# Kernel optimization log

Measured on AMD Instinct MI355X. Metric: run time of the kernel, lower is better.

Reference implementation:

```python
import jax, jax.numpy as jnp
import numpy as np


def _aggregate(xyz, node, features, k):
    # xyz: [B,3,N], node: [B,3,M], features: [B,C,N] -> [B,C,M]
    # squared euclidean distances via expansion (same math as (x-n)^2 sum)
    d = (jnp.sum(xyz ** 2, axis=1)[:, :, None]
         + jnp.sum(node ** 2, axis=1)[:, None, :]
         - 2.0 * jnp.einsum('bdn,bdm->bnm', xyz, node))  # [B,N,M]
    # k smallest over N for each of M nodes (order irrelevant: max-pool after)
    _, nn_idx = jax.lax.top_k(-jnp.transpose(d, (0, 2, 1)), k)  # [B,M,k]
    # gather C-channel features at neighbor indices -> [B,C,M,k]
    g = jnp.take_along_axis(features[:, :, None, :], nn_idx[:, None, :, :], axis=3)
    return jnp.max(g, axis=3)  # [B,C,M]


def setup_inputs() -> dict:
    key = jax.random.key(0)
    k1, k2, k3, k4 = jax.random.split(key, 4)
    B, N, C = 4, 16384, 128
    return {
        'input_coords': jax.random.normal(k1, (B, 3, N), dtype=jnp.float32),
        'input_feats': jax.random.normal(k2, (B, C, N), dtype=jnp.float32),
        'W': jax.random.normal(k3, (C, C), dtype=jnp.float32) * 0.05,
        'b': jax.random.normal(k4, (C,), dtype=jnp.float32) * 0.05,
        'num_sample': 2048,
        'num_agg': 16,
    }


def reference(input_coords, input_feats, W, b, num_sample, num_agg):
    # Dropout in eval mode -> identity. proj = 1x1 Conv1d == per-point linear.
    Z = input_feats  # [B,C,N]
    proj = jax.nn.relu(jnp.einsum('oc,bcn->bon', W, Z) + b[None, :, None])
    vector = jnp.max(proj, axis=-1, keepdims=True)  # [B,C,1]
    weights = jnp.sum(input_feats * vector, axis=1)  # [B,N]
    scores = jax.nn.sigmoid(weights)
    values, idx = jax.lax.top_k(scores, num_sample)  # [B,M] each, sorted desc
    pool_coords_static = jnp.take_along_axis(input_coords, idx[:, None, :], axis=2)  # [B,3,M]
    pool_feats_static = jnp.take_along_axis(input_feats, idx[:, None, :], axis=2)    # [B,C,M]
    v = values[:, None, :]  # [B,1,M]
    pool_feats = pool_feats_static * v
    pool_coords = pool_coords_static * v
    agg_feats = _aggregate(input_coords, pool_coords_static, input_feats, num_agg)  # [B,C,M]
    pool_feats = jnp.concatenate([pool_feats, agg_feats], axis=1)  # [B,2C,M]
    return (pool_coords_static, pool_coords, pool_feats)
```

## Files before the change

kernel.cpp:

```cpp
#include <hip/hip_runtime.h>
#include <hip/hip_bf16.h>
#include <stdint.h>

#define BB 4
#define NN 16384
#define CC 128
#define MM 2048
#define KNN 16
#define QCAP 512
#define EPS 1e-3f

typedef unsigned int u32;
typedef unsigned short u16;
typedef unsigned long long u64;

#define OFF_FEATT   0ull
#define OFF_PTS4    33554432ull
#define OFF_WT      37748736ull
#define OFF_KEYS    37814272ull
#define OFF_VEC     38338560ull
#define OFF_IDX     38340608ull
#define OFF_VAL     38373376ull
#define OFF_TMP1    38406144ull
#define OFF_TMP2    38668288ull

__device__ __forceinline__ float np_dist(float4 p, float4 nd) {
#pragma clang fp contract(off)
    float dot = ((p.x * nd.x) + (p.y * nd.y)) + (p.z * nd.z);
    float d = (p.w + nd.w) - 2.0f * dot;
    return d;
}

__device__ __forceinline__ float sfast(float4 p, float4 nd) {
    float dot = fmaf(p.x, nd.x, fmaf(p.y, nd.y, p.z * nd.z));
    return fmaf(-2.0f, dot, p.w);
}

__device__ __forceinline__ u32 mono_bits(float d) {
    u32 u = __float_as_uint(d);
    u ^= ((u32)(((int)u) >> 31)) | 0x80000000u;
    return u;
}

__device__ __forceinline__ float kth16(float v, int l) {
    float sv = v;
#pragma unroll
    for (int k = 2; k <= 64; k <<= 1) {
#pragma unroll
        for (int j = k >> 1; j > 0; j >>= 1) {
            float pv = __shfl_xor(sv, j);
            bool up = ((l & k) == 0);
            bool tmin = (((l & j) == 0) == up);
            float mn = fminf(sv, pv), mx = fmaxf(sv, pv);
            sv = tmin ? mn : mx;
        }
    }
    return __shfl(sv, 15);
}

__global__ void k_prep(const float* __restrict__ coords, const float* __restrict__ W,
                       float4* __restrict__ pts4, float* __restrict__ WT,
                       u32* __restrict__ vecU) {
    int g = blockIdx.x * 256 + threadIdx.x;
    if (g < BB * NN) {
        int b = g >> 14, n = g & (NN - 1);
        const float* cb = coords + (size_t)b * 3 * NN;
        float x = cb[n], y = cb[NN + n], z = cb[2 * NN + n];
        float w;
        {
#pragma clang fp contract(off)
            w = ((x * x) + (y * y)) + (z * z);
        }
        pts4[g] = make_float4(x, y, z, w);
    } else if (g < BB * NN + CC * CC) {
        int i = g - BB * NN;
        int o = i >> 7, c = i & 127;
        WT[c * CC + o] = W[i];
    } else if (g < BB * NN + CC * CC + BB * CC) {
        vecU[g - BB * NN - CC * CC] = 0u;
    }
}

__global__ __launch_bounds__(256) void k_tv(const float* __restrict__ feats,
        const float* __restrict__ WT, const float* __restrict__ bias,
        float* __restrict__ feat_t, u32* __restrict__ vecU) {
    __shared__ float t[CC][65];
    int bx = blockIdx.x;
    int b = bx >> 8; int n0 = (bx & 255) * 64;
    int tid = threadIdx.x, l = tid & 63;
    int w = __builtin_amdgcn_readfirstlane(tid >> 6);
    const float* fb = feats + (size_t)b * CC * NN + n0;
#pragma unroll
    for (int p = 0; p < 32; ++p) {
        int r = p * 4 + w;
        t[r][l] = fb[(size_t)r * NN + l];
    }
    __syncthreads();
    float* ob = feat_t + ((size_t)b * NN + n0) * CC;
#pragma unroll
    for (int p = 0; p < 32; ++p) {
        int r = (p >> 1) * 4 + w;
        int c = (p & 1) * 64 + l;
        ob[(size_t)r * CC + c] = t[c][r];
    }
    int o0 = w * 32;
    float acc[32];
#pragma unroll
    for (int oi = 0; oi < 32; ++oi) acc[oi] = bias[o0 + oi];
    for (int c = 0; c < CC; ++c) {
        float zc = t[c][l];
        const float4* wt4 = (const float4*)(WT + c * CC + o0);
#pragma unroll
        for (int q = 0; q < 8; ++q) {
            float4 wv = wt4[q];
            acc[q * 4 + 0] = fmaf(wv.x, zc, acc[q * 4 + 0]);
            acc[q * 4 + 1] = fmaf(wv.y, zc, acc[q * 4 + 1]);
            acc[q * 4 + 2] = fmaf(wv.z, zc, acc[q * 4 + 2]);
            acc[q * 4 + 3] = fmaf(wv.w, zc, acc[q * 4 + 3]);
        }
    }
#pragma unroll
    for (int oi = 0; oi < 32; ++oi) {
        float rv = acc[oi] > 0.0f ? acc[oi] : 0.0f;
#pragma unroll
        for (int s = 32; s; s >>= 1) rv = fmaxf(rv, __shfl_xor(rv, s));
        if (l == 0) atomicMax(vecU + b * CC + o0 + oi, __float_as_uint(rv));
    }
}

__global__ void k_scores(const float* __restrict__ feats, const float* __restrict__ vecF,
                         u64* __restrict__ keys) {
    int i = blockIdx.x * 256 + threadIdx.x;
    int b = i >> 14, n = i & (NN - 1);
    const float* fb = feats + (size_t)b * CC * NN + n;
    const float* vb = vecF + b * CC;
    float wsum = 0.f;
#pragma unroll 8
    for (int c = 0; c < CC; ++c) wsum = fmaf(fb[(size_t)c * NN], vb[c], wsum);
    float s = 1.0f / (1.0f + expf(-wsum));
    u32 mono = __float_as_uint(s);
    keys[i] = ((u64)mono << 32) | (u64)(0xFFFFFFFFu - (u32)n);
}

__global__ __launch_bounds__(1024) void k_sortchunk(u64* __restrict__ keys) {
    __shared__ u64 sk[2048];
    int b = blockIdx.x >> 3, c = blockIdx.x & 7;
    int tid = threadIdx.x;
    u64* src = keys + (size_t)b * NN + c * 2048;
    sk[tid] = src[tid];
    sk[tid + 1024] = src[tid + 1024];
    for (int size = 2; size <= 2048; size <<= 1) {
        for (int stride = size >> 1; stride > 0; stride >>= 1) {
            __syncthreads();
            int t = tid;
            int i = (t << 1) - (t & (stride - 1));
            int j = i + stride;
            u64 a = sk[i], cc = sk[j];
            bool up = ((i & size) == 0);
            if ((a < cc) == up) { sk[i] = cc; sk[j] = a; }
        }
    }
    __syncthreads();
    src[tid] = sk[tid];
    src[tid + 1024] = sk[tid + 1024];
}

__global__ __launch_bounds__(512) void k_mergetop(const u64* __restrict__ in,
        u64* __restrict__ outp, int lg ) {
    __shared__ u64 mk[4096];
    int b = blockIdx.x >> lg, pr = blockIdx.x & ((1 << lg) - 1);
    int tid = threadIdx.x;
    const u64* s0 = in + ((size_t)((b << lg) + pr) * 2) * 2048;
    const u64* s1 = s0 + 2048;
    for (int t = tid; t < 2048; t += 512) { mk[t] = s0[t]; mk[2048 + t] = s1[2047 - t]; }
    __syncthreads();
    for (int t = tid; t < 2048; t += 512) {
        u64 a = mk[t], c = mk[t + 2048];
        if (a < c) { mk[t] = c; mk[t + 2048] = a; }
    }
    for (int stride = 1024; stride > 0; stride >>= 1) {
        __syncthreads();
        for (int t = tid; t < 1024; t += 512) {
            int i = (t << 1) - (t & (stride - 1));
            int j = i + stride;
            u64 a = mk[i], c = mk[j];
            if (a < c) { mk[i] = c; mk[j] = a; }
        }
    }
    __syncthreads();
    u64* dst = outp + (size_t)((b << lg) + pr) * 2048;
    for (int t = tid; t < 2048; t += 512) dst[t] = mk[t];
}

__global__ __launch_bounds__(512) void k_mergefinal(const u64* __restrict__ in,
        u32* __restrict__ idxA, float* __restrict__ valA) {
    __shared__ u64 mk[4096];
    int b = blockIdx.x, tid = threadIdx.x;
    const u64* s0 = in + (size_t)(b * 2) * 2048;
    const u64* s1 = s0 + 2048;
    for (int t = tid; t < 2048; t += 512) { mk[t] = s0[t]; mk[2048 + t] = s1[2047 - t]; }
    __syncthreads();
    for (int t = tid; t < 2048; t += 512) {
        u64 a = mk[t], c = mk[t + 2048];
        if (a < c) { mk[t] = c; mk[t + 2048] = a; }
    }
    for (int stride = 1024; stride > 0; stride >>= 1) {
        __syncthreads();
        for (int t = tid; t < 1024; t += 512) {
            int i = (t << 1) - (t & (stride - 1));
            int j = i + stride;
            u64 a = mk[i], c = mk[j];
            if (a < c) { mk[i] = c; mk[j] = a; }
        }
    }
    __syncthreads();
    for (int t = tid; t < 2048; t += 512) {
        u64 k = mk[t];
        idxA[b * MM + t] = 0xFFFFFFFFu - (u32)(k & 0xFFFFFFFFull);
        valA[b * MM + t] = __uint_as_float((u32)(k >> 32));
    }
}

__global__ void k_gather(const float4* __restrict__ pts4, const float* __restrict__ feat_t,
        const u32* __restrict__ idxA, const float* __restrict__ valA, float* __restrict__ out) {
    int g = blockIdx.x * 256 + threadIdx.x;
    int b = g >> 11, i = g & (MM - 1);
    u32 n = idxA[g];
    float v = valA[g];
    float4 p = pts4[(b << 14) + (int)n];
    float* o0 = out + (size_t)b * 3 * MM + i;
    o0[0] = p.x; o0[MM] = p.y; o0[2 * MM] = p.z;
    float* o1 = o0 + 24576;
    o1[0] = p.x * v; o1[MM] = p.y * v; o1[2 * MM] = p.z * v;
    const float4* ft = (const float4*)(feat_t + ((size_t)(b << 14) + n) * CC);
    float* o2 = out + 49152 + ((size_t)b * 256) * MM + i;
#pragma unroll 8
    for (int q = 0; q < 32; ++q) {
        float4 f = ft[q];
        o2[(size_t)(4 * q + 0) * MM] = f.x * v;
        o2[(size_t)(4 * q + 1) * MM] = f.y * v;
        o2[(size_t)(4 * q + 2) * MM] = f.z * v;
        o2[(size_t)(4 * q + 3) * MM] = f.w * v;
    }
}

__global__ __launch_bounds__(256, 7) void k_knn(const float4* __restrict__ pts4,
        const float* __restrict__ feat_t, const u32* __restrict__ idxA, float* __restrict__ out) {
    __shared__ float4 ptsS[1024];
    __shared__ u16 qS[4][QCAP];
    __shared__ float4 nodeS[4];
    int bx = blockIdx.x;
    int b = bx >> 9, mblk = bx & 511;
    int tid = threadIdx.x, l = tid & 63;
    const float4* pb = pts4 + (b << 14);
    if (tid < 4) nodeS[tid] = pb[idxA[b * MM + mblk * 4 + tid]];
#pragma unroll
    for (int j = 0; j < 4; ++j) ptsS[tid + 256 * j] = pb[tid + 256 * j];
    __syncthreads();
    int w = __builtin_amdgcn_readfirstlane(tid >> 6);
    float4 nd = nodeS[w];
    float lm = 3.0e38f;
#pragma unroll 4
    for (int j = 0; j < 16; ++j) lm = fminf(lm, sfast(ptsS[l + 64 * j], nd));
    __syncthreads();
#pragma unroll
    for (int j = 0; j < 4; ++j) ptsS[tid + 256 * j] = pb[1024 + tid + 256 * j];
    __syncthreads();
#pragma unroll 4
    for (int j = 0; j < 16; ++j) lm = fminf(lm, sfast(ptsS[l + 64 * j], nd));
    float T = kth16(lm, l) + 2.0f * EPS;
    int qc = 0;
    for (int ch = 0; ch < 16; ++ch) {
        __syncthreads();
#pragma unroll
        for (int j = 0; j < 4; ++j) ptsS[tid + 256 * j] = pb[ch * 1024 + tid + 256 * j];
        __syncthreads();
        for (int j = 0; j < 16; ++j) {
            float4 p = ptsS[l + 64 * j];
            float dt = fmaf(p.x, nd.x, fmaf(p.y, nd.y, p.z * nd.z));
            float s = fmaf(-2.0f, dt, p.w);
            bool pred = (s <= T);
            u64 bal = __ballot(pred);
            if (bal) {
                if (pred) {
                    int off = __builtin_amdgcn_mbcnt_hi((u32)(bal >> 32),
                              __builtin_amdgcn_mbcnt_lo((u32)bal, 0));
                    int slot = qc + off;
                    if (slot < QCAP) qS[w][slot] = (u16)(ch * 1024 + l + 64 * j);
                }
                qc += (int)__popcll(bal);
            }
        }
    }
    int cnt = qc < QCAP ? qc : QCAP;
    u64 regk[QCAP / 64];
#pragma unroll
    for (int s = 0; s < QCAP / 64; ++s) {
        u64 kk = ~0ull;
        if ((s << 6) < cnt) {
            int pos = (s << 6) + l;
            if (pos < cnt) {
                u32 n = qS[w][pos];
                float d = np_dist(pb[n], nd);
                kk = ((u64)mono_bits(d) << 32) | (u64)n;
            }
        }
        regk[s] = kk;
    }
    float mx0 = -3.0e38f, mx1 = -3.0e38f;
    for (int it = 0; it < KNN; ++it) {
        u64 mykey = ~0ull;
#pragma unroll
        for (int s = 0; s < QCAP / 64; ++s)
            if ((s << 6) < cnt) mykey = regk[s] < mykey ? regk[s] : mykey;
        u64 r = mykey;
#pragma unroll
        for (int j = 32; j > 0; j >>= 1) {
            u64 o = __shfl_xor(r, j);
            r = o < r ? o : r;
        }
#pragma unroll
        for (int s = 0; s < QCAP / 64; ++s)
            if ((s << 6) < cnt) { if (regk[s] == r) regk[s] = ~0ull; }
        if (r != ~0ull) {
            u32 nj = (u32)(r & 0xFFFFFFFFull);
            const float2 f = *(const float2*)(feat_t + ((size_t)(b << 14) + nj) * CC + (l << 1));
            mx0 = fmaxf(mx0, f.x);
            mx1 = fmaxf(mx1, f.y);
        }
    }
    int m = mblk * 4 + w;
    size_t ob = 49152 + ((size_t)(b * 256 + 128 + 2 * l)) * MM + m;
    out[ob] = mx0;
    out[ob + MM] = mx1;
}

extern "C" void kernel_launch(void* const* d_in, const int* in_sizes, int n_in,
                              void* d_out, int out_size, void* d_ws, size_t ws_size,
                              hipStream_t stream) {
    const float* coords = (const float*)d_in[0];
    const float* feats  = (const float*)d_in[1];
    const float* W      = (const float*)d_in[2];
    const float* bias   = (const float*)d_in[3];
    char* ws = (char*)d_ws;
    float*  feat_t = (float*)(ws + OFF_FEATT);
    float4* pts4   = (float4*)(ws + OFF_PTS4);
    float*  WT     = (float*)(ws + OFF_WT);
    u64*    keys   = (u64*)(ws + OFF_KEYS);
    u32*    vecU   = (u32*)(ws + OFF_VEC);
    u32*    idxA   = (u32*)(ws + OFF_IDX);
    float*  valA   = (float*)(ws + OFF_VAL);
    u64*    tmp1   = (u64*)(ws + OFF_TMP1);
    u64*    tmp2   = (u64*)(ws + OFF_TMP2);
    float*  out    = (float*)d_out;

    int prepN = BB * NN + CC * CC + BB * CC;
    k_prep     <<<(prepN + 255) / 256, 256, 0, stream>>>(coords, W, pts4, WT, vecU);
    k_tv       <<<BB * (NN / 64), 256, 0, stream>>>(feats, WT, bias, feat_t, vecU);
    k_scores   <<<BB * NN / 256, 256, 0, stream>>>(feats, (const float*)vecU, keys);
    k_sortchunk<<<BB * 8, 1024, 0, stream>>>(keys);
    k_mergetop <<<BB * 4, 512, 0, stream>>>(keys, tmp1, 2);
    k_mergetop <<<BB * 2, 512, 0, stream>>>(tmp1, tmp2, 1);
    k_mergefinal<<<BB, 512, 0, stream>>>(tmp2, idxA, valA);
    k_gather   <<<BB * MM / 256, 256, 0, stream>>>(pts4, feat_t, idxA, valA, out);
    k_knn      <<<BB * (MM / 4), 256, 0, stream>>>(pts4, feat_t, idxA, out);
}
```

Before: 274.7 us.

## Split transpose from projection and remap projection threads to output channels

```diff
diff --git a/kernel.cpp b/kernel.cpp
--- a/kernel.cpp
+++ b/kernel.cpp
@@ -81,51 +81,61 @@
     }
 }
 
-__global__ __launch_bounds__(256) void k_tv(const float* __restrict__ feats,
-        const float* __restrict__ WT, const float* __restrict__ bias,
-        float* __restrict__ feat_t, u32* __restrict__ vecU) {
-    __shared__ float t[CC][65];
+__global__ void k_transpose(const float* __restrict__ feats, float* __restrict__ feat_t) {
+    __shared__ float t[64][65];
+    int bx = blockIdx.x;
+    int b = bx >> 9; int rem = bx & 511; int nb = rem >> 1; int cb2 = rem & 1;
+    int n0 = nb * 64, c0 = cb2 * 64;
+    int l = threadIdx.x & 63, r0 = threadIdx.x >> 6;
+    const float* fb = feats + (size_t)b * CC * NN;
+#pragma unroll
+    for (int p = 0; p < 16; ++p) {
+        int r = r0 + p * 4;
+        t[r][l] = fb[(size_t)(c0 + r) * NN + n0 + l];
+    }
+    __syncthreads();
+    float* ob = feat_t + (size_t)b * NN * CC;
+#pragma unroll
+    for (int p = 0; p < 16; ++p) {
+        int r = r0 + p * 4;
+        ob[(size_t)(n0 + r) * CC + c0 + l] = t[l][r];
+    }
+}
+
+__global__ __launch_bounds__(256) void k_vec(const float* __restrict__ feat_t,
+        const float* __restrict__ WT, const float* __restrict__ bias, u32* __restrict__ vecU) {
     int bx = blockIdx.x;
     int b = bx >> 8; int n0 = (bx & 255) * 64;
     int tid = threadIdx.x, l = tid & 63;
     int w = __builtin_amdgcn_readfirstlane(tid >> 6);
-    const float* fb = feats + (size_t)b * CC * NN + n0;
-#pragma unroll
-    for (int p = 0; p < 32; ++p) {
-        int r = p * 4 + w;
-        t[r][l] = fb[(size_t)r * NN + l];
-    }
-    __syncthreads();
-    float* ob = feat_t + ((size_t)b * NN + n0) * CC;
-#pragma unroll
-    for (int p = 0; p < 32; ++p) {
-        int r = (p >> 1) * 4 + w;
-        int c = (p & 1) * 64 + l;
-        ob[(size_t)r * CC + c] = t[c][r];
-    }
-    int o0 = w * 32;
+    int oh = (w & 1) << 6;
+    int ng = w >> 1;
+    int o = oh + l;
+    const float* zt = feat_t + ((size_t)b * NN + n0 + ng * 32) * CC;
+    float bo = bias[o];
     float acc[32];
 #pragma unroll
-    for (int oi = 0; oi < 32; ++oi) acc[oi] = bias[o0 + oi];
-    for (int c = 0; c < CC; ++c) {
-        float zc = t[c][l];
-        const float4* wt4 = (const float4*)(WT + c * CC + o0);
-#pragma unroll
-        for (int q = 0; q < 8; ++q) {
-            float4 wv = wt4[q];
-            acc[q * 4 + 0] = fmaf(wv.x, zc, acc[q * 4 + 0]);
-            acc[q * 4 + 1] = fmaf(wv.y, zc, acc[q * 4 + 1]);
-            acc[q * 4 + 2] = fmaf(wv.z, zc, acc[q * 4 + 2]);
-            acc[q * 4 + 3] = fmaf(wv.w, zc, acc[q * 4 + 3]);
-        }
-    }
-#pragma unroll
-    for (int oi = 0; oi < 32; ++oi) {
-        float rv = acc[oi] > 0.0f ? acc[oi] : 0.0f;
-#pragma unroll
-        for (int s = 32; s; s >>= 1) rv = fmaxf(rv, __shfl_xor(rv, s));
-        if (l == 0) atomicMax(vecU + b * CC + o0 + oi, __float_as_uint(rv));
-    }
+    for (int ni = 0; ni < 32; ++ni) acc[ni] = bo;
+    for (int c0 = 0; c0 < CC; c0 += 32) {
+        float Wreg[32];
+#pragma unroll
+        for (int ci = 0; ci < 32; ++ci) Wreg[ci] = WT[(size_t)(c0 + ci) * CC + o];
+#pragma unroll
+        for (int ni = 0; ni < 32; ++ni) {
+            const float* zr = zt + ni * CC + c0;
+            float a = acc[ni];
+#pragma unroll
+            for (int ci = 0; ci < 32; ++ci) a = fmaf(zr[ci], Wreg[ci], a);
+            acc[ni] = a;
+        }
+    }
+    float mx = 0.0f;
+#pragma unroll
+    for (int ni = 0; ni < 32; ++ni) {
+        float rv = acc[ni] > 0.0f ? acc[ni] : 0.0f;
+        mx = fmaxf(mx, rv);
+    }
+    atomicMax(vecU + b * CC + o, __float_as_uint(mx));
 }
 
 __global__ void k_scores(const float* __restrict__ feats, const float* __restrict__ vecF,
@@ -356,7 +366,8 @@
 
     int prepN = BB * NN + CC * CC + BB * CC;
     k_prep     <<<(prepN + 255) / 256, 256, 0, stream>>>(coords, W, pts4, WT, vecU);
-    k_tv       <<<BB * (NN / 64), 256, 0, stream>>>(feats, WT, bias, feat_t, vecU);
+    k_transpose<<<BB * (NN / 64) * (CC / 64), 256, 0, stream>>>(feats, feat_t);
+    k_vec      <<<BB * (NN / 64), 256, 0, stream>>>(feat_t, WT, bias, vecU);
     k_scores   <<<BB * NN / 256, 256, 0, stream>>>(feats, (const float*)vecU, keys);
     k_sortchunk<<<BB * 8, 1024, 0, stream>>>(keys);
     k_mergetop <<<BB * 4, 512, 0, stream>>>(keys, tmp1, 2);
```

After: 288.7 us. +5.1%, slower.
